# Kernel tuning notes

Measured on AMD Instinct MI355X. Metric: run time of the kernel, lower is better.

The kernel has to match this reference:

```python
import jax, jax.numpy as jnp
import numpy as np

H = 8  # head_number
NEG = -1e30


def setup_inputs() -> dict:
    key = jax.random.key(0)
    ks = jax.random.split(key, 12)
    B, D, L = 32, 1024, 1024
    s = 1.0 / np.sqrt(D)
    x = jax.random.normal(ks[0], (B, D, L), dtype=jnp.float32)
    mask = jax.random.randint(ks[1], (B, L), 0, 2, dtype=jnp.int32)
    wq = jax.random.normal(ks[2], (D, D), dtype=jnp.float32) * s
    bq = jnp.zeros((D,), dtype=jnp.float32)
    wk = jax.random.normal(ks[3], (D, D), dtype=jnp.float32) * s
    bk = jnp.zeros((D,), dtype=jnp.float32)
    wv = jax.random.normal(ks[4], (D, D), dtype=jnp.float32) * s
    bv = jnp.zeros((D,), dtype=jnp.float32)
    wo = jax.random.normal(ks[5], (D, D), dtype=jnp.float32) * s
    bo = jnp.zeros((D,), dtype=jnp.float32)
    return {"x": x, "mask": mask, "wq": wq, "bq": bq, "wk": wk, "bk": bk,
            "wv": wv, "bv": bv, "wo": wo, "bo": bo}


def reference(x, mask, wq, bq, wk, bk, wv, bv, wo, bo):
    # x: [B, D, L]; mask: [B, L] with 1 = masked (pad). Dropout in eval mode (identity).
    B, D, L = x.shape
    dh = D // H
    scale = 1.0 / np.sqrt(dh)
    xt = jnp.swapaxes(x, 1, 2)  # [B, L, D]
    q = (xt @ wq.T + bq).reshape(B, L, H, dh)
    k = (xt @ wk.T + bk).reshape(B, L, H, dh)
    v = (xt @ wv.T + bv).reshape(B, L, H, dh)
    scores = jnp.einsum('bqhd,bkhd->bhqk', q, k) * scale  # [B, H, L, L]
    m = mask.astype(scores.dtype)[:, None, None, :]  # broadcast over heads, query pos
    scores = scores * (1.0 - m) + m * NEG
    attn = jax.nn.softmax(scores, axis=-1)
    out = jnp.einsum('bhqk,bkhd->bqhd', attn, v).reshape(B, L, D)
    out = out @ wo.T + bo
    return jnp.swapaxes(out, 1, 2)  # [B, D, L]
```

## Files before the change

kernel.cpp:

```cpp
#include <hip/hip_runtime.h>
#include <hip/hip_bf16.h>

typedef __bf16 bf16_t;
typedef bf16_t bf16x8 __attribute__((ext_vector_type(8)));
typedef float f32x4 __attribute__((ext_vector_type(4)));

#define MFMA16(a, b, c) __builtin_amdgcn_mfma_f32_16x16x32_bf16(a, b, c, 0, 0, 0)
#define NEGV -1e30f

__device__ __forceinline__ unsigned short f2bf(float f) {
  union { float f; unsigned int u; } v; v.f = f;
  unsigned int r = v.u + 0x7FFFu + ((v.u >> 16) & 1u);
  return (unsigned short)(r >> 16);
}

__device__ __forceinline__ void gload16(const unsigned short* g, unsigned short* l) {
  __builtin_amdgcn_global_load_lds(
      (const __attribute__((address_space(1))) void*)g,
      (__attribute__((address_space(3))) void*)l, 16, 0, 0);
}

__global__ __launch_bounds__(256) void x_transpose(
    const float* __restrict__ x, unsigned short* __restrict__ xT)
{
  const int b = blockIdx.z;
  const int l0 = blockIdx.x * 64, d0 = blockIdx.y * 64;
  __shared__ __align__(16) unsigned short T[64][68];
  const int tid = threadIdx.x;
  const int dl = tid >> 4, lc = (tid & 15) * 4;
#pragma unroll
  for (int rep = 0; rep < 4; ++rep) {
    int d = dl + rep * 16;
    float4 v = *reinterpret_cast<const float4*>(
        x + ((size_t)b * 1024 + d0 + d) * 1024 + l0 + lc);
    ushort4 u;
    u.x = f2bf(v.x); u.y = f2bf(v.y); u.z = f2bf(v.z); u.w = f2bf(v.w);
    *reinterpret_cast<ushort4*>(&T[d][lc]) = u;
  }
  __syncthreads();
  const int dbase = (tid & 15) * 4, lbase = (tid >> 4) * 4;
  ushort4 r0 = *reinterpret_cast<const ushort4*>(&T[dbase + 0][lbase]);
  ushort4 r1 = *reinterpret_cast<const ushort4*>(&T[dbase + 1][lbase]);
  ushort4 r2 = *reinterpret_cast<const ushort4*>(&T[dbase + 2][lbase]);
  ushort4 r3 = *reinterpret_cast<const ushort4*>(&T[dbase + 3][lbase]);
  ushort4 w0 = {r0.x, r1.x, r2.x, r3.x};
  ushort4 w1 = {r0.y, r1.y, r2.y, r3.y};
  ushort4 w2 = {r0.z, r1.z, r2.z, r3.z};
  ushort4 w3 = {r0.w, r1.w, r2.w, r3.w};
  unsigned short* op = xT + ((size_t)b * 1024 + l0 + lbase) * 1024 + d0 + dbase;
  *reinterpret_cast<ushort4*>(op) = w0;
  *reinterpret_cast<ushort4*>(op + 1024) = w1;
  *reinterpret_cast<ushort4*>(op + 2048) = w2;
  *reinterpret_cast<ushort4*>(op + 3072) = w3;
}

__global__ __launch_bounds__(256) void w_convert(
    const float* __restrict__ wq, const float* __restrict__ wk,
    const float* __restrict__ wv, const float* __restrict__ wo,
    unsigned short* __restrict__ Wqkv, unsigned short* __restrict__ Wo)
{
  const int z = blockIdx.y;
  const float* src = (z == 0) ? wq : (z == 1) ? wk : (z == 2) ? wv : wo;
  unsigned short* dst = (z < 3) ? Wqkv + (size_t)z * 1048576 : Wo;
  size_t off = ((size_t)blockIdx.x * 256 + threadIdx.x) * 4;
  float4 v = *reinterpret_cast<const float4*>(src + off);
  ushort4 u = {f2bf(v.x), f2bf(v.y), f2bf(v.z), f2bf(v.w)};
  *reinterpret_cast<ushort4*>(dst + off) = u;
}

__global__ __launch_bounds__(512, 2) void qkv_gemm8(
    const unsigned short* __restrict__ xT, const unsigned short* __restrict__ Wqkv,
    const float* __restrict__ bq, const float* __restrict__ bk, const float* __restrict__ bv,
    unsigned short* __restrict__ Q, unsigned short* __restrict__ K,
    unsigned short* __restrict__ Vt)
{
  __shared__ __align__(16) unsigned short lds[2][4][8192];

  const int tid = threadIdx.x;
  const int wave = tid >> 6, lane = tid & 63;
  const int lr = lane & 15, lg = lane >> 4;
  const int wr = wave >> 2, wc = wave & 3;

  const int bid = blockIdx.x;
  const int swz = (bid & 7) * 192 + (bid >> 3);
  const int mt = swz / 12, nt = swz % 12;
  const int m0 = mt * 256, n0 = nt * 256;

  const unsigned short* Ag = xT + (size_t)m0 * 1024;
  const unsigned short* Bg = Wqkv + (size_t)n0 * 1024;

  const int srow = tid >> 2;
  const int schk = (tid & 3) * 8;

#define STAGE_HT(BUF, REG, TI)                                                 \
  {                                                                            \
    const int kt_ = ((TI) < 16 ? (TI) : 15) * 64 + (((REG)&1) * 32) + schk;    \
    const unsigned short* gp_ = (((REG) < 2) ? Ag : Bg);                       \
    _Pragma("unroll")                                                          \
    for (int j_ = 0; j_ < 2; ++j_)                                             \
      gload16(gp_ + (size_t)(j_ * 128 + srow) * 1024 + kt_,                    \
              &lds[BUF][REG][j_ * 4096 + tid * 8]);                            \
  }

#define LDA(BUF, KK, MH, AR)                                                   \
  _Pragma("unroll")                                                            \
  for (int mi_ = 0; mi_ < 4; ++mi_)                                            \
    AR[mi_] = *reinterpret_cast<const bf16x8*>(                                \
        &lds[BUF][KK][(wr * 128 + (MH)*64 + mi_ * 16 + lr) * 32 + lg * 8]);

#define LDB(BUF, KK, BR)                                                       \
  _Pragma("unroll")                                                            \
  for (int n_ = 0; n_ < 4; ++n_)                                               \
    BR[n_] = *reinterpret_cast<const bf16x8*>(                                 \
        &lds[BUF][2 + (KK)][(wc * 64 + n_ * 16 + lr) * 32 + lg * 8]);

#define MM(AR, BR, MH)                                                         \
  __builtin_amdgcn_s_setprio(1);                                               \
  _Pragma("unroll")                                                            \
  for (int mi_ = 0; mi_ < 4; ++mi_)                                            \
    _Pragma("unroll")                                                          \
    for (int n_ = 0; n_ < 4; ++n_)                                             \
      acc[(MH)*4 + mi_][n_] = MFMA16(AR[mi_], BR[n_], acc[(MH)*4 + mi_][n_]);  \
  __builtin_amdgcn_s_setprio(0);

#define BAR()                                                                  \
  {                                                                            \
    asm volatile("" ::: "memory");                                             \
    __builtin_amdgcn_s_barrier();                                              \
    asm volatile("" ::: "memory");                                             \
  }
#define VMW() asm volatile("s_waitcnt vmcnt(10)" ::: "memory")

  f32x4 acc[8][4];
#pragma unroll
  for (int m = 0; m < 8; ++m)
#pragma unroll
    for (int n = 0; n < 4; ++n) acc[m][n] = (f32x4){0.f, 0.f, 0.f, 0.f};

  STAGE_HT(0, 2, 0); STAGE_HT(0, 0, 0); STAGE_HT(0, 3, 0); STAGE_HT(0, 1, 0);
  STAGE_HT(1, 2, 1); STAGE_HT(1, 0, 1); STAGE_HT(1, 3, 1);
  VMW();
  BAR();

  for (int it = 0; it < 8; ++it) {
    const int T = 2 * it;
    bf16x8 a0[4], a1[4], b0[4], b1[4];
    LDB(0, 0, b0); LDA(0, 0, 0, a0);
    STAGE_HT(1, 1, T + 1);
    BAR();
    MM(a0, b0, 0);
    BAR();
    LDA(0, 0, 1, a1);
    STAGE_HT(0, 2, T + 2);
    BAR();
    MM(a1, b0, 1);
    VMW(); BAR();
    LDB(0, 1, b1); LDA(0, 1, 0, a0);
    STAGE_HT(0, 0, T + 2);
    BAR();
    MM(a0, b1, 0);
    BAR();
    LDA(0, 1, 1, a1);
    STAGE_HT(0, 3, T + 2);
    BAR();
    MM(a1, b1, 1);
    VMW(); BAR();
    LDB(1, 0, b0); LDA(1, 0, 0, a0);
    STAGE_HT(0, 1, T + 2);
    BAR();
    MM(a0, b0, 0);
    BAR();
    LDA(1, 0, 1, a1);
    STAGE_HT(1, 2, T + 3);
    BAR();
    MM(a1, b0, 1);
    VMW(); BAR();
    LDB(1, 1, b1); LDA(1, 1, 0, a0);
    STAGE_HT(1, 0, T + 3);
    BAR();
    MM(a0, b1, 0);
    BAR();
    LDA(1, 1, 1, a1);
    STAGE_HT(1, 3, T + 3);
    BAR();
    MM(a1, b1, 1);
    VMW(); BAR();
  }

  const int zi = n0 >> 10;
  const float* bias = (zi == 0) ? bq : (zi == 1) ? bk : bv;
  const int b = m0 >> 10;
  const int lbase = (m0 & 1023) + wr * 128;

  if (zi < 2) {
    unsigned short* op = ((zi == 0) ? Q : K);
#pragma unroll
    for (int n = 0; n < 4; ++n) {
      const int col = (n0 & 1023) + wc * 64 + n * 16 + lr;
      const int h = col >> 7, d = col & 127;
      const float bs = bias[col];
      unsigned short* hp = op + ((size_t)b * 8 + h) * 131072 + d;
#pragma unroll
      for (int m = 0; m < 8; ++m)
#pragma unroll
        for (int ii = 0; ii < 4; ++ii) {
          int l = lbase + m * 16 + lg * 4 + ii;
          hp[(size_t)l * 128] = f2bf(acc[m][n][ii] + bs);
        }
    }
  } else {
#pragma unroll
    for (int n = 0; n < 4; ++n) {
      const int col = (n0 & 1023) + wc * 64 + n * 16 + lr;
      const int h = col >> 7, d = col & 127;
      const float bs = bias[col];
      unsigned short* hp = Vt + ((size_t)b * 8 + h) * 131072 + (size_t)d * 1024;
#pragma unroll
      for (int m = 0; m < 8; ++m) {
        int l = lbase + m * 16 + lg * 4;
        ushort4 u = {f2bf(acc[m][n][0] + bs), f2bf(acc[m][n][1] + bs),
                     f2bf(acc[m][n][2] + bs), f2bf(acc[m][n][3] + bs)};
        *reinterpret_cast<ushort4*>(&hp[l]) = u;
      }
    }
  }
#undef STAGE_HT
}

__global__ __launch_bounds__(512, 2) void out_gemm8(
    const unsigned short* __restrict__ Wo, const unsigned short* __restrict__ O,
    const float* __restrict__ bo, float* __restrict__ out)
{
  __shared__ __align__(16) unsigned short lds[2][4][8192];

  const int tid = threadIdx.x;
  const int wave = tid >> 6, lane = tid & 63;
  const int lr = lane & 15, lg = lane >> 4;
  const int wr = wave >> 2, wc = wave & 3;

  const int b = blockIdx.y;
  const int bid = blockIdx.x;
  const int swz = (bid & 7) * 2 + (bid >> 3);
  const int mt = swz >> 2, nt = swz & 3;
  const int d0 = mt * 256, l0 = nt * 256;

  const unsigned short* Ag = Wo + (size_t)d0 * 1024;
  const unsigned short* Og = O + (size_t)b * 8 * 131072;

  const int srow = tid >> 2;
  const int schk = (tid & 3) * 8;

#define STAGE_HT(BUF, REG, TI)                                                 \
  {                                                                            \
    const int kt_ = ((TI) < 16 ? (TI) : 15) * 64 + (((REG)&1) * 32) + schk;    \
    if ((REG) < 2) {                                                           \
      _Pragma("unroll")                                                        \
      for (int j_ = 0; j_ < 2; ++j_)                                           \
        gload16(Ag + (size_t)(j_ * 128 + srow) * 1024 + kt_,                   \
                &lds[BUF][REG][j_ * 4096 + tid * 8]);                          \
    } else {                                                                   \
      const int h_ = kt_ >> 7, dk_ = kt_ & 127;                                \
      _Pragma("unroll")                                                        \
      for (int j_ = 0; j_ < 2; ++j_)                                           \
        gload16(Og + (size_t)h_ * 131072 +                                     \
                    (size_t)(l0 + j_ * 128 + srow) * 128 + dk_,                \
                &lds[BUF][REG][j_ * 4096 + tid * 8]);                          \
    }                                                                          \
  }

  f32x4 acc[8][4];
#pragma unroll
  for (int m = 0; m < 8; ++m)
#pragma unroll
    for (int n = 0; n < 4; ++n) acc[m][n] = (f32x4){0.f, 0.f, 0.f, 0.f};

  STAGE_HT(0, 2, 0); STAGE_HT(0, 0, 0); STAGE_HT(0, 3, 0); STAGE_HT(0, 1, 0);
  STAGE_HT(1, 2, 1); STAGE_HT(1, 0, 1); STAGE_HT(1, 3, 1);
  VMW();
  BAR();

  for (int it = 0; it < 8; ++it) {
    const int T = 2 * it;
    bf16x8 a0[4], a1[4], b0[4], b1[4];
    LDB(0, 0, b0); LDA(0, 0, 0, a0);
    STAGE_HT(1, 1, T + 1);
    BAR();
    MM(a0, b0, 0);
    BAR();
    LDA(0, 0, 1, a1);
    STAGE_HT(0, 2, T + 2);
    BAR();
    MM(a1, b0, 1);
    VMW(); BAR();
    LDB(0, 1, b1); LDA(0, 1, 0, a0);
    STAGE_HT(0, 0, T + 2);
    BAR();
    MM(a0, b1, 0);
    BAR();
    LDA(0, 1, 1, a1);
    STAGE_HT(0, 3, T + 2);
    BAR();
    MM(a1, b1, 1);
    VMW(); BAR();
    LDB(1, 0, b0); LDA(1, 0, 0, a0);
    STAGE_HT(0, 1, T + 2);
    BAR();
    MM(a0, b0, 0);
    BAR();
    LDA(1, 0, 1, a1);
    STAGE_HT(1, 2, T + 3);
    BAR();
    MM(a1, b0, 1);
    VMW(); BAR();
    LDB(1, 1, b1); LDA(1, 1, 0, a0);
    STAGE_HT(1, 0, T + 3);
    BAR();
    MM(a0, b1, 0);
    BAR();
    LDA(1, 1, 1, a1);
    STAGE_HT(1, 3, T + 3);
    BAR();
    MM(a1, b1, 1);
    VMW(); BAR();
  }

#pragma unroll
  for (int m = 0; m < 8; ++m) {
#pragma unroll
    for (int ii = 0; ii < 4; ++ii) {
      int dr = d0 + wr * 128 + m * 16 + lg * 4 + ii;
      float bs = bo[dr];
      float* orow = out + ((size_t)b * 1024 + dr) * 1024 + l0 + wc * 64 + lr;
#pragma unroll
      for (int n = 0; n < 4; ++n)
        orow[n * 16] = acc[m][n][ii] + bs;
    }
  }
#undef STAGE_HT
#undef LDA
#undef LDB
#undef MM
#undef BAR
#undef VMW
}

__global__ __launch_bounds__(256) void flash_attn(
    const unsigned short* __restrict__ Q, const unsigned short* __restrict__ Kb,
    const unsigned short* __restrict__ Vt, const int* __restrict__ mask,
    unsigned short* __restrict__ O)
{
  const int tid = threadIdx.x, wave = tid >> 6, lane = tid & 63;
  const int lr = lane & 15, lg = lane >> 4;
  const int qt = blockIdx.x, h = blockIdx.y, b = blockIdx.z;
  const size_t bh = (size_t)b * 8 + h;
  const unsigned short* Qp = Q + bh * 131072;
  const unsigned short* Kp = Kb + bh * 131072;
  const unsigned short* Vp = Vt + bh * 131072;
  unsigned short* Op = O + bh * 131072;
  const int q0 = qt * 64 + wave * 16;
  const float SC2 = 0.12751744f;
  const float NEG2 = -1.442695e30f;

  __shared__ __align__(16) unsigned short Kl[2][4096];
  __shared__ __align__(16) unsigned short Vl[2][4096];
  __shared__ __align__(16) unsigned short plds[4][16 * 40];
  __shared__ float pen[1024];

  {
    const int4 mv = *reinterpret_cast<const int4*>(mask + b * 1024 + tid * 4);
    float4 pv;
    pv.x = mv.x ? NEG2 : 0.f; pv.y = mv.y ? NEG2 : 0.f;
    pv.z = mv.z ? NEG2 : 0.f; pv.w = mv.w ? NEG2 : 0.f;
    *reinterpret_cast<float4*>(&pen[tid * 4]) = pv;
  }

  unsigned short* myP = plds[wave];

  bf16x8 aq[4];
#pragma unroll
  for (int c = 0; c < 4; ++c)
    aq[c] = *reinterpret_cast<const bf16x8*>(&Qp[(size_t)(q0 + lr) * 128 + c * 32 + lg * 8]);

#define STAGE(bufi, ktv)                                                        \
  {                                                                             \
    _Pragma("unroll")                                                           \
    for (int i = 0; i < 2; ++i) {                                               \
      int krow = i * 16 + (tid >> 4);                                           \
      int kcb = ((tid & 15) * 16) ^ ((krow & 7) << 4);                          \
      gload16(Kp + (size_t)((ktv) + krow) * 128 + (kcb >> 1),                   \
              &Kl[bufi][i * 2048 + tid * 8]);                                   \
      int aoff = i * 4096 + tid * 16;                                           \
      int r_ = aoff >> 6;                                                       \
      int Lb = aoff ^ (((r_ ^ (r_ >> 2)) & 3) << 4);                            \
      gload16(Vp + (size_t)(Lb >> 6) * 1024 + (ktv) + ((Lb & 63) >> 1),         \
              &Vl[bufi][i * 2048 + tid * 8]);                                   \
    }                                                                           \
  }

  f32x4 oacc[8];
#pragma unroll
  for (int dt = 0; dt < 8; ++dt) oacc[dt] = (f32x4){0.f, 0.f, 0.f, 0.f};
  float mrun = -3.0e38f;
  float lrun = 0.f;

  STAGE(0, 0);
  __syncthreads();

  int cur = 0;
  for (int t = 0; t < 32; ++t) {
    const int kt = t * 32;
    if (t < 31) STAGE(cur ^ 1, kt + 32);

    f32x4 s[2];
    __builtin_amdgcn_s_setprio(1);
#pragma unroll
    for (int n = 0; n < 2; ++n) {
      f32x4 a = (f32x4){0.f, 0.f, 0.f, 0.f};
      const int krow = n * 16 + lr;
      const int rsw = (krow & 7) << 4;
#pragma unroll
      for (int c = 0; c < 4; ++c) {
        bf16x8 bk = *reinterpret_cast<const bf16x8*>(
            &Kl[cur][krow * 128 + (((c * 64 + lg * 16) ^ rsw) >> 1)]);
        a = MFMA16(bk, aq[c], a);
      }
      s[n] = a;
    }
    __builtin_amdgcn_s_setprio(0);

#pragma unroll
    for (int n = 0; n < 2; ++n) {
      f32x4 pv = *reinterpret_cast<const f32x4*>(&pen[kt + n * 16 + lg * 4]);
#pragma unroll
      for (int i = 0; i < 4; ++i) s[n][i] = s[n][i] * SC2 + pv[i];
    }

    float mx = fmaxf(fmaxf(fmaxf(s[0][0], s[0][1]), fmaxf(s[0][2], s[0][3])),
                     fmaxf(fmaxf(s[1][0], s[1][1]), fmaxf(s[1][2], s[1][3])));
    mx = fmaxf(mx, __shfl_xor(mx, 16));
    mx = fmaxf(mx, __shfl_xor(mx, 32));

    if (!__all(mx <= mrun + 8.0f)) {
      float mnew = fmaxf(mrun, mx);
      float scq = __builtin_amdgcn_exp2f(mrun - mnew);
      mrun = mnew;
      lrun *= scq;
#pragma unroll
      for (int i = 0; i < 4; ++i) {
        float sco = __shfl(scq, lg * 4 + i);
#pragma unroll
        for (int dt = 0; dt < 8; ++dt) oacc[dt][i] *= sco;
      }
    }

    float p[2][4];
#pragma unroll
    for (int n = 0; n < 2; ++n)
#pragma unroll
      for (int i = 0; i < 4; ++i)
        p[n][i] = __builtin_amdgcn_exp2f(s[n][i] - mrun);
    float ls = ((p[0][0] + p[0][1]) + (p[0][2] + p[0][3])) +
               ((p[1][0] + p[1][1]) + (p[1][2] + p[1][3]));
    ls += __shfl_xor(ls, 16);
    ls += __shfl_xor(ls, 32);
    lrun += ls;

#pragma unroll
    for (int n = 0; n < 2; ++n)
#pragma unroll
      for (int t2 = 0; t2 < 2; ++t2) {
        unsigned int u;
        asm("v_cvt_pk_bf16_f32 %0, %1, %2"
            : "=v"(u) : "v"(p[n][2 * t2]), "v"(p[n][2 * t2 + 1]));
        *reinterpret_cast<unsigned int*>(
            &myP[lr * 40 + n * 16 + lg * 4 + t2 * 2]) = u;
      }
    bf16x8 pa0 = *reinterpret_cast<const bf16x8*>(&myP[lr * 40 + lg * 8]);

    __builtin_amdgcn_s_setprio(1);
#pragma unroll
    for (int dt = 0; dt < 8; ++dt) {
      const int rr = dt * 16 + lr;
      const int aL = rr * 64 + lg * 16;
      const int ph = aL ^ (((rr ^ (rr >> 2)) & 3) << 4);
      bf16x8 bv = *reinterpret_cast<const bf16x8*>(&Vl[cur][ph >> 1]);
      oacc[dt] = MFMA16(pa0, bv, oacc[dt]);
    }
    __builtin_amdgcn_s_setprio(0);

    __syncthreads();
    cur ^= 1;
  }

  float linv[4];
#pragma unroll
  for (int i = 0; i < 4; ++i) {
    float lq = __shfl(lrun, lg * 4 + i);
    linv[i] = 1.0f / lq;
  }
#pragma unroll
  for (int dt = 0; dt < 8; ++dt)
#pragma unroll
    for (int i = 0; i < 4; ++i)
      Op[(size_t)(q0 + lg * 4 + i) * 128 + dt * 16 + lr] = f2bf(oacc[dt][i] * linv[i]);
#undef STAGE
}

__global__ __launch_bounds__(256) void qkv_proj_old(
    const float* __restrict__ x,
    const float* __restrict__ wq, const float* __restrict__ wk, const float* __restrict__ wv,
    const float* __restrict__ bq, const float* __restrict__ bk, const float* __restrict__ bv,
    unsigned short* __restrict__ Q, unsigned short* __restrict__ K, unsigned short* __restrict__ Vt)
{
  const int tid = threadIdx.x;
  const int wave = tid >> 6, lane = tid & 63;
  const int lr = lane & 15, lg = lane >> 4;
  const int wr = wave >> 1, wc = wave & 1;
  const int mt = blockIdx.x & 7, nt = blockIdx.x >> 3;
  const int b = blockIdx.y, z = blockIdx.z;
  const int l0 = mt * 128, i0 = nt * 128;
  const float* w    = (z == 0) ? wq : (z == 1) ? wk : wv;
  const float* bias = (z == 0) ? bq : (z == 1) ? bk : bv;
  unsigned short* outp = (z == 0) ? Q : (z == 1) ? K : Vt;

  __shared__ __align__(16) unsigned short lA[128 * 40];
  __shared__ __align__(16) unsigned short lB[128 * 40];

  f32x4 acc[4][4];
#pragma unroll
  for (int m = 0; m < 4; ++m)
#pragma unroll
    for (int n = 0; n < 4; ++n) acc[m][n] = (f32x4){0.f, 0.f, 0.f, 0.f};

  const int ad = tid >> 3, aj = tid & 7;
  const int br = tid >> 1, bh2 = tid & 1;

  for (int k0 = 0; k0 < 1024; k0 += 32) {
    const float* xp = x + ((size_t)b * 1024 + k0 + ad) * 1024 + l0;
#pragma unroll
    for (int rep = 0; rep < 4; ++rep) {
      float4 v = *reinterpret_cast<const float4*>(xp + aj * 4 + rep * 32);
      int lb = aj * 4 + rep * 32;
      lA[(lb + 0) * 40 + ad] = f2bf(v.x);
      lA[(lb + 1) * 40 + ad] = f2bf(v.y);
      lA[(lb + 2) * 40 + ad] = f2bf(v.z);
      lA[(lb + 3) * 40 + ad] = f2bf(v.w);
    }
    const float* wp = w + (size_t)(i0 + br) * 1024 + k0 + bh2 * 16;
#pragma unroll
    for (int rep = 0; rep < 4; ++rep) {
      float4 v = *reinterpret_cast<const float4*>(wp + rep * 4);
      int cb = br * 40 + bh2 * 16 + rep * 4;
      lB[cb + 0] = f2bf(v.x); lB[cb + 1] = f2bf(v.y);
      lB[cb + 2] = f2bf(v.z); lB[cb + 3] = f2bf(v.w);
    }
    __syncthreads();
    bf16x8 af[4], bfr[4];
#pragma unroll
    for (int m = 0; m < 4; ++m)
      af[m] = *reinterpret_cast<const bf16x8*>(&lA[(wr * 64 + m * 16 + lr) * 40 + lg * 8]);
#pragma unroll
    for (int n = 0; n < 4; ++n)
      bfr[n] = *reinterpret_cast<const bf16x8*>(&lB[(wc * 64 + n * 16 + lr) * 40 + lg * 8]);
#pragma unroll
    for (int m = 0; m < 4; ++m)
#pragma unroll
      for (int n = 0; n < 4; ++n)
        acc[m][n] = MFMA16(af[m], bfr[n], acc[m][n]);
    __syncthreads();
  }
#pragma unroll
  for (int n = 0; n < 4; ++n) {
    int col = i0 + wc * 64 + n * 16 + lr;
    float bs = bias[col];
    int h = col >> 7, d = col & 127;
#pragma unroll
    for (int m = 0; m < 4; ++m) {
#pragma unroll
      for (int ii = 0; ii < 4; ++ii) {
        int row = l0 + wr * 64 + m * 16 + lg * 4 + ii;
        unsigned short val = f2bf(acc[m][n][ii] + bs);
        if (z < 2)
          outp[(((size_t)b * 8 + h) * 1024 + row) * 128 + d] = val;
        else
          outp[(((size_t)b * 8 + h) * 128 + d) * 1024 + row] = val;
      }
    }
  }
}

__global__ __launch_bounds__(256) void out_proj_old(
    const unsigned short* __restrict__ Obuf, const float* __restrict__ wo,
    const float* __restrict__ bo, float* __restrict__ out)
{
  const int tid = threadIdx.x, wave = tid >> 6, lane = tid & 63;
  const int lr = lane & 15, lg = lane >> 4;
  const int wr = wave >> 1, wc = wave & 1;
  const int mt = blockIdx.x & 7, nt = blockIdx.x >> 3;
  const int b = blockIdx.y;
  const int d0 = mt * 128, l0 = nt * 128;

  __shared__ __align__(16) unsigned short lA[128 * 40];
  __shared__ __align__(16) unsigned short lB[128 * 40];

  f32x4 acc[4][4];
#pragma unroll
  for (int m = 0; m < 4; ++m)
#pragma unroll
    for (int n = 0; n < 4; ++n) acc[m][n] = (f32x4){0.f, 0.f, 0.f, 0.f};

  const int ar = tid >> 1, ah = tid & 1;

  for (int k0 = 0; k0 < 1024; k0 += 32) {
    const float* wp = wo + (size_t)(d0 + ar) * 1024 + k0 + ah * 16;
#pragma unroll
    for (int rep = 0; rep < 4; ++rep) {
      float4 v = *reinterpret_cast<const float4*>(wp + rep * 4);
      int cb = ar * 40 + ah * 16 + rep * 4;
      lA[cb + 0] = f2bf(v.x); lA[cb + 1] = f2bf(v.y);
      lA[cb + 2] = f2bf(v.z); lA[cb + 3] = f2bf(v.w);
    }
    {
      int head = k0 >> 7, dk = (k0 & 127) + ah * 16;
      const unsigned short* op =
          Obuf + (((size_t)b * 8 + head) * 1024 + l0 + ar) * 128 + dk;
#pragma unroll
      for (int rep = 0; rep < 2; ++rep) {
        bf16x8 v = *reinterpret_cast<const bf16x8*>(op + rep * 8);
        *reinterpret_cast<bf16x8*>(&lB[ar * 40 + ah * 16 + rep * 8]) = v;
      }
    }
    __syncthreads();
    bf16x8 af[4], bfr[4];
#pragma unroll
    for (int m = 0; m < 4; ++m)
      af[m] = *reinterpret_cast<const bf16x8*>(&lA[(wr * 64 + m * 16 + lr) * 40 + lg * 8]);
#pragma unroll
    for (int n = 0; n < 4; ++n)
      bfr[n] = *reinterpret_cast<const bf16x8*>(&lB[(wc * 64 + n * 16 + lr) * 40 + lg * 8]);
#pragma unroll
    for (int m = 0; m < 4; ++m)
#pragma unroll
      for (int n = 0; n < 4; ++n)
        acc[m][n] = MFMA16(af[m], bfr[n], acc[m][n]);
    __syncthreads();
  }
#pragma unroll
  for (int m = 0; m < 4; ++m) {
#pragma unroll
    for (int ii = 0; ii < 4; ++ii) {
      int dr = d0 + wr * 64 + m * 16 + lg * 4 + ii;
      float bs = bo[dr];
      float* orow = out + ((size_t)b * 1024 + dr) * 1024 + l0 + wc * 64 + lr;
#pragma unroll
      for (int n = 0; n < 4; ++n)
        orow[n * 16] = acc[m][n][ii] + bs;
    }
  }
}

extern "C" void kernel_launch(void* const* d_in, const int* in_sizes, int n_in,
                              void* d_out, int out_size, void* d_ws, size_t ws_size,
                              hipStream_t stream) {
  const float* x  = (const float*)d_in[0];
  const int* mask = (const int*)d_in[1];
  const float* wq = (const float*)d_in[2];
  const float* bq = (const float*)d_in[3];
  const float* wk = (const float*)d_in[4];
  const float* bk = (const float*)d_in[5];
  const float* wv = (const float*)d_in[6];
  const float* bv = (const float*)d_in[7];
  const float* wo = (const float*)d_in[8];
  const float* bo = (const float*)d_in[9];
  float* out = (float*)d_out;

  const size_t MB64 = (size_t)64 << 20;
  const size_t NEED = (size_t)264 << 20;

  if (ws_size >= NEED) {
    unsigned short* xT   = (unsigned short*)d_ws;
    unsigned short* Q    = (unsigned short*)((char*)d_ws + MB64);
    unsigned short* K    = (unsigned short*)((char*)d_ws + 2 * MB64);
    unsigned short* Vt   = (unsigned short*)((char*)d_ws + 3 * MB64);
    unsigned short* Wqkv = (unsigned short*)((char*)d_ws + 4 * MB64);
    unsigned short* Wo   = Wqkv + (size_t)3 * 1048576;

    x_transpose<<<dim3(16, 16, 32), 256, 0, stream>>>(x, xT);
    w_convert<<<dim3(1024, 4), 256, 0, stream>>>(wq, wk, wv, wo, Wqkv, Wo);
    qkv_gemm8<<<dim3(1536), 512, 0, stream>>>(xT, Wqkv, bq, bk, bv, Q, K, Vt);
    flash_attn<<<dim3(16, 8, 32), 256, 0, stream>>>(Q, K, Vt, mask, Q);
    out_gemm8<<<dim3(16, 32), 512, 0, stream>>>(Wo, Q, bo, out);
  } else {
    unsigned short* Q  = (unsigned short*)d_ws;
    unsigned short* K  = Q + (size_t)33554432;
    unsigned short* Vt = K + (size_t)33554432;
    qkv_proj_old<<<dim3(64, 32, 3), 256, 0, stream>>>(x, wq, wk, wv, bq, bk, bv, Q, K, Vt);
    flash_attn<<<dim3(16, 8, 32), 256, 0, stream>>>(Q, K, Vt, mask, Q);
    out_proj_old<<<dim3(64, 32), 256, 0, stream>>>(Q, wo, bo, out);
  }
}
```

Measured before the change: 652.4 us.

## Enlarge flash-attention tiles to 128 queries and 64 keys per iteration

```diff
diff --git a/kernel.cpp b/kernel.cpp
--- a/kernel.cpp
+++ b/kernel.cpp
@@ -344,7 +344,7 @@
 #undef VMW
 }
 
-__global__ __launch_bounds__(256) void flash_attn(
+__global__ __launch_bounds__(256, 2) void flash_attn(
     const unsigned short* __restrict__ Q, const unsigned short* __restrict__ Kb,
     const unsigned short* __restrict__ Vt, const int* __restrict__ mask,
     unsigned short* __restrict__ O)
@@ -357,13 +357,13 @@
   const unsigned short* Kp = Kb + bh * 131072;
   const unsigned short* Vp = Vt + bh * 131072;
   unsigned short* Op = O + bh * 131072;
-  const int q0 = qt * 64 + wave * 16;
+  const int q0 = qt * 128 + wave * 32;
   const float SC2 = 0.12751744f;
   const float NEG2 = -1.442695e30f;
 
-  __shared__ __align__(16) unsigned short Kl[2][4096];
-  __shared__ __align__(16) unsigned short Vl[2][4096];
-  __shared__ __align__(16) unsigned short plds[4][16 * 40];
+  __shared__ __align__(16) unsigned short Kl[2][64 * 128];
+  __shared__ __align__(16) unsigned short Vl[2][128 * 64];
+  __shared__ __align__(16) unsigned short plds[4][16 * 76];
   __shared__ float pen[1024];
 
   {
@@ -376,134 +376,162 @@
 
   unsigned short* myP = plds[wave];
 
-  bf16x8 aq[4];
-#pragma unroll
-  for (int c = 0; c < 4; ++c)
-    aq[c] = *reinterpret_cast<const bf16x8*>(&Qp[(size_t)(q0 + lr) * 128 + c * 32 + lg * 8]);
+  bf16x8 aq0[4], aq1[4];
+#pragma unroll
+  for (int c = 0; c < 4; ++c) {
+    aq0[c] = *reinterpret_cast<const bf16x8*>(
+        &Qp[(size_t)(q0 + lr) * 128 + c * 32 + lg * 8]);
+    aq1[c] = *reinterpret_cast<const bf16x8*>(
+        &Qp[(size_t)(q0 + 16 + lr) * 128 + c * 32 + lg * 8]);
+  }
 
 #define STAGE(bufi, ktv)                                                        \
   {                                                                             \
     _Pragma("unroll")                                                           \
-    for (int i = 0; i < 2; ++i) {                                               \
+    for (int i = 0; i < 4; ++i) {                                               \
       int krow = i * 16 + (tid >> 4);                                           \
       int kcb = ((tid & 15) * 16) ^ ((krow & 7) << 4);                          \
       gload16(Kp + (size_t)((ktv) + krow) * 128 + (kcb >> 1),                   \
               &Kl[bufi][i * 2048 + tid * 8]);                                   \
       int aoff = i * 4096 + tid * 16;                                           \
-      int r_ = aoff >> 6;                                                       \
-      int Lb = aoff ^ (((r_ ^ (r_ >> 2)) & 3) << 4);                            \
-      gload16(Vp + (size_t)(Lb >> 6) * 1024 + (ktv) + ((Lb & 63) >> 1),         \
+      int r_ = aoff >> 7;                                                       \
+      int Lb = aoff ^ ((r_ & 7) << 4);                                          \
+      gload16(Vp + (size_t)r_ * 1024 + (ktv) + ((Lb & 127) >> 1),               \
               &Vl[bufi][i * 2048 + tid * 8]);                                   \
     }                                                                           \
   }
 
-  f32x4 oacc[8];
-#pragma unroll
-  for (int dt = 0; dt < 8; ++dt) oacc[dt] = (f32x4){0.f, 0.f, 0.f, 0.f};
-  float mrun = -3.0e38f;
-  float lrun = 0.f;
+#define SMAXPV(S, MR, LRN, OA)                                                  \
+  {                                                                             \
+    float mx = fmaxf(                                                           \
+        fmaxf(fmaxf(fmaxf(S[0][0], S[0][1]), fmaxf(S[0][2], S[0][3])),          \
+              fmaxf(fmaxf(S[1][0], S[1][1]), fmaxf(S[1][2], S[1][3]))),         \
+        fmaxf(fmaxf(fmaxf(S[2][0], S[2][1]), fmaxf(S[2][2], S[2][3])),          \
+              fmaxf(fmaxf(S[3][0], S[3][1]), fmaxf(S[3][2], S[3][3]))));        \
+    mx = fmaxf(mx, __shfl_xor(mx, 16));                                         \
+    mx = fmaxf(mx, __shfl_xor(mx, 32));                                         \
+    if (!__all(mx <= MR + 8.0f)) {                                              \
+      float mnew = fmaxf(MR, mx);                                               \
+      float scq = __builtin_amdgcn_exp2f(MR - mnew);                            \
+      MR = mnew;                                                                \
+      LRN *= scq;                                                               \
+      _Pragma("unroll")                                                         \
+      for (int i = 0; i < 4; ++i) {                                             \
+        float sco = __shfl(scq, lg * 4 + i);                                    \
+        _Pragma("unroll")                                                       \
+        for (int dt = 0; dt < 8; ++dt) OA[dt][i] *= sco;                        \
+      }                                                                         \
+    }                                                                           \
+    float p_[4][4];                                                             \
+    float ls = 0.f;                                                             \
+    _Pragma("unroll")                                                           \
+    for (int n = 0; n < 4; ++n) {                                               \
+      _Pragma("unroll")                                                         \
+      for (int i = 0; i < 4; ++i)                                               \
+        p_[n][i] = __builtin_amdgcn_exp2f(S[n][i] - MR);                        \
+      ls += (p_[n][0] + p_[n][1]) + (p_[n][2] + p_[n][3]);                      \
+    }                                                                           \
+    ls += __shfl_xor(ls, 16);                                                   \
+    ls += __shfl_xor(ls, 32);                                                   \
+    LRN += ls;                                                                  \
+    _Pragma("unroll")                                                           \
+    for (int n = 0; n < 4; ++n)                                                 \
+      _Pragma("unroll")                                                         \
+      for (int t2 = 0; t2 < 2; ++t2) {                                          \
+        unsigned int u_;                                                        \
+        asm("v_cvt_pk_bf16_f32 %0, %1, %2"                                      \
+            : "=v"(u_) : "v"(p_[n][2 * t2]), "v"(p_[n][2 * t2 + 1]));           \
+        *reinterpret_cast<unsigned int*>(                                       \
+            &myP[lr * 76 + n * 16 + lg * 4 + t2 * 2]) = u_;                     \
+      }                                                                         \
+    bf16x8 pa0_ = *reinterpret_cast<const bf16x8*>(&myP[lr * 76 + lg * 8]);     \
+    bf16x8 pa1_ = *reinterpret_cast<const bf16x8*>(&myP[lr * 76 + 32 + lg * 8]);\
+    __builtin_amdgcn_s_setprio(1);                                              \
+    _Pragma("unroll")                                                           \
+    for (int dt = 0; dt < 8; ++dt) {                                            \
+      const int rr = dt * 16 + lr;                                              \
+      const int rsw_ = (rr & 7) << 4;                                           \
+      bf16x8 bv0 = *reinterpret_cast<const bf16x8*>(                            \
+          &Vl[cur][(rr * 128 + ((lg * 16) ^ rsw_)) >> 1]);                      \
+      bf16x8 bv1 = *reinterpret_cast<const bf16x8*>(                            \
+          &Vl[cur][(rr * 128 + ((64 + lg * 16) ^ rsw_)) >> 1]);                 \
+      OA[dt] = MFMA16(pa0_, bv0, OA[dt]);                                       \
+      OA[dt] = MFMA16(pa1_, bv1, OA[dt]);                                       \
+    }                                                                           \
+    __builtin_amdgcn_s_setprio(0);                                              \
+  }
+
+  f32x4 oacc0[8], oacc1[8];
+#pragma unroll
+  for (int dt = 0; dt < 8; ++dt) {
+    oacc0[dt] = (f32x4){0.f, 0.f, 0.f, 0.f};
+    oacc1[dt] = (f32x4){0.f, 0.f, 0.f, 0.f};
+  }
+  float mrun0 = -3.0e38f, lrun0 = 0.f;
+  float mrun1 = -3.0e38f, lrun1 = 0.f;
 
   STAGE(0, 0);
   __syncthreads();
 
   int cur = 0;
-  for (int t = 0; t < 32; ++t) {
-    const int kt = t * 32;
-    if (t < 31) STAGE(cur ^ 1, kt + 32);
-
-    f32x4 s[2];
+  for (int t = 0; t < 16; ++t) {
+    const int kt = t * 64;
+    if (t < 15) STAGE(cur ^ 1, kt + 64);
+
+    f32x4 s0[4], s1[4];
     __builtin_amdgcn_s_setprio(1);
 #pragma unroll
-    for (int n = 0; n < 2; ++n) {
-      f32x4 a = (f32x4){0.f, 0.f, 0.f, 0.f};
+    for (int n = 0; n < 4; ++n) {
       const int krow = n * 16 + lr;
       const int rsw = (krow & 7) << 4;
+      f32x4 a0 = (f32x4){0.f, 0.f, 0.f, 0.f};
+      f32x4 a1 = (f32x4){0.f, 0.f, 0.f, 0.f};
 #pragma unroll
       for (int c = 0; c < 4; ++c) {
         bf16x8 bk = *reinterpret_cast<const bf16x8*>(
             &Kl[cur][krow * 128 + (((c * 64 + lg * 16) ^ rsw) >> 1)]);
-        a = MFMA16(bk, aq[c], a);
+        a0 = MFMA16(bk, aq0[c], a0);
+        a1 = MFMA16(bk, aq1[c], a1);
       }
-      s[n] = a;
+      s0[n] = a0;
+      s1[n] = a1;
     }
     __builtin_amdgcn_s_setprio(0);
 
 #pragma unroll
-    for (int n = 0; n < 2; ++n) {
+    for (int n = 0; n < 4; ++n) {
       f32x4 pv = *reinterpret_cast<const f32x4*>(&pen[kt + n * 16 + lg * 4]);
 #pragma unroll
-      for (int i = 0; i < 4; ++i) s[n][i] = s[n][i] * SC2 + pv[i];
-    }
-
-    float mx = fmaxf(fmaxf(fmaxf(s[0][0], s[0][1]), fmaxf(s[0][2], s[0][3])),
-                     fmaxf(fmaxf(s[1][0], s[1][1]), fmaxf(s[1][2], s[1][3])));
-    mx = fmaxf(mx, __shfl_xor(mx, 16));
-    mx = fmaxf(mx, __shfl_xor(mx, 32));
-
-    if (!__all(mx <= mrun + 8.0f)) {
-      float mnew = fmaxf(mrun, mx);
-      float scq = __builtin_amdgcn_exp2f(mrun - mnew);
-      mrun = mnew;
-      lrun *= scq;
-#pragma unroll
       for (int i = 0; i < 4; ++i) {
-        float sco = __shfl(scq, lg * 4 + i);
-#pragma unroll
-        for (int dt = 0; dt < 8; ++dt) oacc[dt][i] *= sco;
+        s0[n][i] = s0[n][i] * SC2 + pv[i];
+        s1[n][i] = s1[n][i] * SC2 + pv[i];
       }
     }
 
-    float p[2][4];
-#pragma unroll
-    for (int n = 0; n < 2; ++n)
-#pragma unroll
-      for (int i = 0; i < 4; ++i)
-        p[n][i] = __builtin_amdgcn_exp2f(s[n][i] - mrun);
-    float ls = ((p[0][0] + p[0][1]) + (p[0][2] + p[0][3])) +
-               ((p[1][0] + p[1][1]) + (p[1][2] + p[1][3]));
-    ls += __shfl_xor(ls, 16);
-    ls += __shfl_xor(ls, 32);
-    lrun += ls;
-
-#pragma unroll
-    for (int n = 0; n < 2; ++n)
-#pragma unroll
-      for (int t2 = 0; t2 < 2; ++t2) {
-        unsigned int u;
-        asm("v_cvt_pk_bf16_f32 %0, %1, %2"
-            : "=v"(u) : "v"(p[n][2 * t2]), "v"(p[n][2 * t2 + 1]));
-        *reinterpret_cast<unsigned int*>(
-            &myP[lr * 40 + n * 16 + lg * 4 + t2 * 2]) = u;
-      }
-    bf16x8 pa0 = *reinterpret_cast<const bf16x8*>(&myP[lr * 40 + lg * 8]);
-
-    __builtin_amdgcn_s_setprio(1);
-#pragma unroll
-    for (int dt = 0; dt < 8; ++dt) {
-      const int rr = dt * 16 + lr;
-      const int aL = rr * 64 + lg * 16;
-      const int ph = aL ^ (((rr ^ (rr >> 2)) & 3) << 4);
-      bf16x8 bv = *reinterpret_cast<const bf16x8*>(&Vl[cur][ph >> 1]);
-      oacc[dt] = MFMA16(pa0, bv, oacc[dt]);
-    }
-    __builtin_amdgcn_s_setprio(0);
+    SMAXPV(s0, mrun0, lrun0, oacc0);
+    SMAXPV(s1, mrun1, lrun1, oacc1);
 
     __syncthreads();
     cur ^= 1;
   }
 
-  float linv[4];
+  float linv0[4], linv1[4];
 #pragma unroll
   for (int i = 0; i < 4; ++i) {
-    float lq = __shfl(lrun, lg * 4 + i);
-    linv[i] = 1.0f / lq;
+    linv0[i] = 1.0f / __shfl(lrun0, lg * 4 + i);
+    linv1[i] = 1.0f / __shfl(lrun1, lg * 4 + i);
   }
 #pragma unroll
   for (int dt = 0; dt < 8; ++dt)
 #pragma unroll
-    for (int i = 0; i < 4; ++i)
-      Op[(size_t)(q0 + lg * 4 + i) * 128 + dt * 16 + lr] = f2bf(oacc[dt][i] * linv[i]);
+    for (int i = 0; i < 4; ++i) {
+      Op[(size_t)(q0 + lg * 4 + i) * 128 + dt * 16 + lr] =
+          f2bf(oacc0[dt][i] * linv0[i]);
+      Op[(size_t)(q0 + 16 + lg * 4 + i) * 128 + dt * 16 + lr] =
+          f2bf(oacc1[dt][i] * linv1[i]);
+    }
 #undef STAGE
+#undef SMAXPV
 }
 
 __global__ __launch_bounds__(256) void qkv_proj_old(
@@ -688,14 +716,14 @@
     x_transpose<<<dim3(16, 16, 32), 256, 0, stream>>>(x, xT);
     w_convert<<<dim3(1024, 4), 256, 0, stream>>>(wq, wk, wv, wo, Wqkv, Wo);
     qkv_gemm8<<<dim3(1536), 512, 0, stream>>>(xT, Wqkv, bq, bk, bv, Q, K, Vt);
-    flash_attn<<<dim3(16, 8, 32), 256, 0, stream>>>(Q, K, Vt, mask, Q);
+    flash_attn<<<dim3(8, 8, 32), 256, 0, stream>>>(Q, K, Vt, mask, Q);
     out_gemm8<<<dim3(16, 32), 512, 0, stream>>>(Wo, Q, bo, out);
   } else {
     unsigned short* Q  = (unsigned short*)d_ws;
     unsigned short* K  = Q + (size_t)33554432;
     unsigned short* Vt = K + (size_t)33554432;
     qkv_proj_old<<<dim3(64, 32, 3), 256, 0, stream>>>(x, wq, wk, wv, bq, bk, bv, Q, K, Vt);
-    flash_attn<<<dim3(16, 8, 32), 256, 0, stream>>>(Q, K, Vt, mask, Q);
+    flash_attn<<<dim3(8, 8, 32), 256, 0, stream>>>(Q, K, Vt, mask, Q);
     out_proj_old<<<dim3(64, 32), 256, 0, stream>>>(Q, wo, bo, out);
   }
 }
```

Result: faster. 600.9 us (-7.9%).
